# Kernel tuning notes

Measured on AMD Instinct MI355X. Metric: run time of the kernel, lower is better.

The kernel has to match this reference:

```python
import jax, jax.numpy as jnp
import numpy as np

IN_F = 2048
OUT_F = 2048
N_ROWS = 8192


def _perm(n):
    # t_o(n) is a permutation matrix P with P[i, p(i)] = 1, p(i) = (4i mod n) + (4i // n)
    i = np.arange(n)
    return (4 * i) % n + (4 * i) // n


def _inv(p):
    inv = np.empty_like(p)
    inv[p] = np.arange(len(p))
    return inv

# (P_in^T @ H)[a, :] = H[i, :] where p_in(i) = a  ->  rows indexed by inv(p_in)
_INV_P_IN = _inv(_perm(IN_F))
# (H @ P_out)[:, b] = H[:, j] where p_out(j) = b  ->  cols indexed by inv(p_out)
_INV_P_OUT = _inv(_perm(OUT_F))


def make_quaternion_mul(kernel):
    # kernel: (in//4, out); split along dim 1 into quaternion components
    r, i, j, k = jnp.split(kernel, 4, axis=1)
    r2 = jnp.concatenate([r, -i, -j, -k], axis=1)
    i2 = jnp.concatenate([i, r, -k, j], axis=1)
    j2 = jnp.concatenate([j, k, r, -i], axis=1)
    k2 = jnp.concatenate([k, -j, i, r], axis=1)
    return jnp.concatenate([r2, i2, j2, k2], axis=0)  # (in, out)


def setup_inputs() -> dict:
    key = jax.random.key(0)
    k1, k2, k3 = jax.random.split(key, 3)
    inp = jax.random.normal(k1, (N_ROWS, IN_F), dtype=jnp.float32)
    weight = jax.random.normal(k2, (IN_F // 4, OUT_F), dtype=jnp.float32) * (1.0 / np.sqrt(IN_F // 4))
    bias = jax.random.normal(k3, (OUT_F,), dtype=jnp.float32) * 0.01
    return {"input": inp, "weight": weight, "bias": bias}


def reference(input, weight, bias):
    hamilton = make_quaternion_mul(weight)                 # (in, out)
    # swap=True: hamilton = L^T @ hamilton @ R, both pure permutations
    hamilton = hamilton[_INV_P_IN][:, _INV_P_OUT]
    support = input @ hamilton + bias[None, :]             # (N, out)
    return support
```

## Files before the change

### kernel.cpp

```cpp
#include <hip/hip_runtime.h>
#include <stdint.h>

#define IN_F 2048
#define OUT_F 2048
#define N_ROWS 8192

#define BM 256
#define BN 256
#define BK 32
#define NT (IN_F / BK)
#define TM_TILES (N_ROWS / BM)
#define TN_TILES (OUT_F / BN)
#define NWG (TM_TILES * TN_TILES)
#define TILE_SHORTS (BM * BK)
#define BUF_SHORTS (2 * TILE_SHORTS)

typedef __bf16 bf16x8 __attribute__((ext_vector_type(8)));
typedef float f32x4 __attribute__((ext_vector_type(4)));
typedef unsigned short ushortx8 __attribute__((ext_vector_type(8)));

__device__ __forceinline__ unsigned short f2bf(float f) {
  unsigned u = __builtin_bit_cast(unsigned, f);
  u += 0x7FFFu + ((u >> 16) & 1u);
  return (unsigned short)(u >> 16);
}

__device__ __forceinline__ void async16(void* lds, const void* g) {
  __builtin_amdgcn_global_load_lds(
      (const __attribute__((address_space(1))) void*)(uintptr_t)g,
      (__attribute__((address_space(3))) void*)(uint32_t)(uintptr_t)lds,
      16, 0, 0);
}

__device__ __forceinline__ bf16x8 ld8(const unsigned short* p) {
  return __builtin_bit_cast(bf16x8, *reinterpret_cast<const ushortx8*>(p));
}

__global__ __launch_bounds__(256) void k_prep(const float* __restrict__ A,
                                              unsigned short* __restrict__ Ab,
                                              const float* __restrict__ W,
                                              unsigned short* __restrict__ Ht) {
  const int bid = blockIdx.x;
  if (bid < 8192) {
    const size_t t = (size_t)bid * 256 + threadIdx.x;
    const float4* a4 = reinterpret_cast<const float4*>(A);
    float4 v0 = a4[2 * t];
    float4 v1 = a4[2 * t + 1];
    ushortx8 o;
    o[0] = f2bf(v0.x); o[1] = f2bf(v0.y); o[2] = f2bf(v0.z); o[3] = f2bf(v0.w);
    o[4] = f2bf(v1.x); o[5] = f2bf(v1.y); o[6] = f2bf(v1.z); o[7] = f2bf(v1.w);
    *reinterpret_cast<ushortx8*>(Ab + t * 8) = o;
  } else {
    const int t = (bid - 8192) * 256 + threadIdx.x;
    const int b = t >> 8;
    const int a0 = (t & 255) << 3;
    const int c = b & 3, v = b >> 2;
    ushortx8 o;
#pragma unroll
    for (int e = 0; e < 8; ++e) {
      const int a = a0 + e;
      const int q = a & 3, u = a >> 2;
      float w = W[(size_t)u * OUT_F + ((q ^ c) << 9) + v];
      if ((0x284E >> ((q << 2) | c)) & 1) w = -w;
      o[e] = f2bf(w);
    }
    *reinterpret_cast<ushortx8*>(Ht + (size_t)b * IN_F + a0) = o;
  }
}

__global__ __launch_bounds__(512, 2) void k_gemm(const unsigned short* __restrict__ A,
                                                 const unsigned short* __restrict__ Bt,
                                                 const float* __restrict__ bias,
                                                 float* __restrict__ C) {
  __shared__ __align__(16) unsigned short lds[4 * BUF_SHORTS];

  const int tid = threadIdx.x;
  const int lane = tid & 63;
  const int w = tid >> 6;
  const int wm = w >> 2;
  const int wn = w & 3;
  const int fr = lane & 15;
  const int g = lane >> 4;

  const int wg = blockIdx.x;
  const int swz = (wg & 7) * (NWG >> 3) + (wg >> 3);
  const int tm = swz >> 3;
  const int tn = swz & 7;
  const int row0 = tm * BM, col0 = tn * BN;

  const unsigned short* srcA[2];
  const unsigned short* srcB[2];
  int tOff[2];
#pragma unroll
  for (int i = 0; i < 2; ++i) {
    const int t = w * 128 + i * 64 + lane;
    const int r = t >> 2, s = t & 3;
    const int ga = s ^ ((r >> 1) & 3);
    srcA[i] = A + (size_t)(row0 + r) * IN_F + ga * 8;
    srcB[i] = Bt + (size_t)(col0 + r) * IN_F + ga * 8;
    tOff[i] = t * 8;
  }

#define STAGE(T)                                              \
  do {                                                        \
    unsigned short* base_ = &lds[((T) & 3) * BUF_SHORTS];     \
    const int ko_ = (T) * BK;                                 \
    async16(base_ + tOff[0], srcA[0] + ko_);                  \
    async16(base_ + tOff[1], srcA[1] + ko_);                  \
    async16(base_ + TILE_SHORTS + tOff[0], srcB[0] + ko_);    \
    async16(base_ + TILE_SHORTS + tOff[1], srcB[1] + ko_);    \
  } while (0)

  int offA[8], offB[4];
#pragma unroll
  for (int m = 0; m < 8; ++m) {
    const int r = wm * 128 + m * 16 + fr;
    offA[m] = r * BK + (g ^ ((r >> 1) & 3)) * 8;
  }
#pragma unroll
  for (int n = 0; n < 4; ++n) {
    const int r = wn * 64 + n * 16 + fr;
    offB[n] = r * BK + (g ^ ((r >> 1) & 3)) * 8;
  }

  f32x4 acc[8][4] = {};

#define MFMA_(a_, b_, c_) __builtin_amdgcn_mfma_f32_16x16x32_bf16(a_, b_, c_, 0, 0, 0)
#define FENCE_ __builtin_amdgcn_sched_barrier(0)

  STAGE(0);
  STAGE(1);
  STAGE(2);

#define TILE(T, VMSTR, DOSTAGE)                                               \
  do {                                                                        \
    asm volatile("s_waitcnt vmcnt(" VMSTR ")" ::: "memory");                  \
    __builtin_amdgcn_s_barrier();                                             \
    FENCE_;                                                                   \
    const unsigned short* ab_ = &lds[((T) & 3) * BUF_SHORTS];                 \
    const unsigned short* bb_ = ab_ + TILE_SHORTS;                            \
    bf16x8 bg[4], af0[4], af1[4];                                             \
    _Pragma("unroll") for (int n = 0; n < 4; ++n) bg[n] = ld8(bb_ + offB[n]); \
    _Pragma("unroll") for (int m = 0; m < 4; ++m) af0[m] = ld8(ab_ + offA[m]);\
    FENCE_;                                                                   \
    if (DOSTAGE) STAGE((T) + 3);                                              \
    _Pragma("unroll") for (int m = 0; m < 4; ++m)                             \
        af1[m] = ld8(ab_ + offA[4 + m]);                                      \
    FENCE_;                                                                   \
    __builtin_amdgcn_s_setprio(1);                                            \
    _Pragma("unroll") for (int n = 0; n < 4; ++n)                             \
        _Pragma("unroll") for (int m = 0; m < 4; ++m)                         \
            acc[m][n] = MFMA_(af0[m], bg[n], acc[m][n]);                      \
    __builtin_amdgcn_s_setprio(0);                                            \
    FENCE_;                                                                   \
    __builtin_amdgcn_s_setprio(1);                                            \
    _Pragma("unroll") for (int n = 0; n < 4; ++n)                             \
        _Pragma("unroll") for (int m = 0; m < 4; ++m)                         \
            acc[4 + m][n] = MFMA_(af1[m], bg[n], acc[4 + m][n]);              \
    __builtin_amdgcn_s_setprio(0);                                            \
    FENCE_;                                                                   \
  } while (0)

  for (int t = 0; t < NT - 3; ++t) {
    TILE(t, "8", true);
  }
  TILE(NT - 3, "8", false);
  TILE(NT - 2, "4", false);
  TILE(NT - 1, "0", false);

#undef TILE
#undef STAGE

  const int g4 = g << 2;
  float bv[4];
#pragma unroll
  for (int n = 0; n < 4; ++n) bv[n] = bias[col0 + wn * 64 + n * 16 + fr];
#pragma unroll
  for (int m = 0; m < 8; ++m) {
#pragma unroll
    for (int e = 0; e < 4; ++e) {
      const int row = row0 + wm * 128 + m * 16 + g4 + e;
      float* cp = C + (size_t)row * OUT_F + col0 + wn * 64 + fr;
#pragma unroll
      for (int n = 0; n < 4; ++n) cp[n * 16] = acc[m][n][e] + bv[n];
    }
  }
}

__global__ __launch_bounds__(256) void k_naive(const float* __restrict__ A,
                                               const float* __restrict__ W,
                                               const float* __restrict__ bias,
                                               float* __restrict__ C) {
  const int idx = blockIdx.x * 256 + threadIdx.x;
  const int m = idx >> 11;
  const int b = idx & (OUT_F - 1);
  const int c = b & 3, v = b >> 2;
  float acc = 0.f;
  const float* arow = A + (size_t)m * IN_F;
  for (int a = 0; a < IN_F; ++a) {
    const int q = a & 3, u = a >> 2;
    float h = W[(size_t)u * OUT_F + ((q ^ c) << 9) + v];
    if ((0x284E >> ((q << 2) | c)) & 1) h = -h;
    acc += arow[a] * h;
  }
  C[idx] = acc + bias[b];
}

extern "C" void kernel_launch(void* const* d_in, const int* in_sizes, int n_in,
                              void* d_out, int out_size, void* d_ws, size_t ws_size,
                              hipStream_t stream) {
  (void)in_sizes; (void)n_in; (void)out_size;
  const float* inp  = (const float*)d_in[0];
  const float* w    = (const float*)d_in[1];
  const float* bias = (const float*)d_in[2];
  float* out = (float*)d_out;

  const size_t needA = (size_t)N_ROWS * IN_F * sizeof(unsigned short);
  const size_t needH = (size_t)IN_F * OUT_F * sizeof(unsigned short);
  if (ws_size < needA + needH) {
    k_naive<<<(N_ROWS * OUT_F) / 256, 256, 0, stream>>>(inp, w, bias, out);
    return;
  }

  unsigned short* Ab = (unsigned short*)d_ws;
  unsigned short* Ht = Ab + (size_t)N_ROWS * IN_F;

  k_prep<<<8192 + 2048, 256, 0, stream>>>(inp, Ab, w, Ht);
  k_gemm<<<NWG, 512, 0, stream>>>(Ab, Ht, bias, out);
}
```

Baseline: 97.15 us.

## Restructure GEMM main loop into BK=64 ping-pong with interleaved half-tile staging

Doubles the K tile to 64 and replaces the 4-deep ring of small stages with two LDS buffers. Each iteration reads fragments in quarter-M slices and issues the next tile's A/B halves between them, using a new 8-way XOR swizzle for the wider rows. Barriers separate every read/MFMA phase so that global loads overlap compute at a finer grain. The trade is many more workgroup barriers per iteration and a shallower prefetch, which could expose memory latency.

```diff
diff --git a/kernel.cpp b/kernel.cpp
--- a/kernel.cpp
+++ b/kernel.cpp
@@ -7,13 +7,13 @@
 
 #define BM 256
 #define BN 256
-#define BK 32
+#define BK 64
 #define NT (IN_F / BK)
 #define TM_TILES (N_ROWS / BM)
 #define TN_TILES (OUT_F / BN)
 #define NWG (TM_TILES * TN_TILES)
-#define TILE_SHORTS (BM * BK)
-#define BUF_SHORTS (2 * TILE_SHORTS)
+#define AB_STRIDE 32768
+#define B_OFF 16384
 
 typedef __bf16 bf16x8 __attribute__((ext_vector_type(8)));
 typedef float f32x4 __attribute__((ext_vector_type(4)));
@@ -72,7 +72,7 @@
                                                  const unsigned short* __restrict__ Bt,
                                                  const float* __restrict__ bias,
                                                  float* __restrict__ C) {
-  __shared__ __align__(16) unsigned short lds[4 * BUF_SHORTS];
+  __shared__ __align__(16) unsigned short lds[2 * AB_STRIDE];
 
   const int tid = threadIdx.x;
   const int lane = tid & 63;
@@ -88,88 +88,111 @@
   const int tn = swz & 7;
   const int row0 = tm * BM, col0 = tn * BN;
 
-  const unsigned short* srcA[2];
-  const unsigned short* srcB[2];
-  int tOff[2];
-#pragma unroll
-  for (int i = 0; i < 2; ++i) {
-    const int t = w * 128 + i * 64 + lane;
-    const int r = t >> 2, s = t & 3;
-    const int ga = s ^ ((r >> 1) & 3);
-    srcA[i] = A + (size_t)(row0 + r) * IN_F + ga * 8;
-    srcB[i] = Bt + (size_t)(col0 + r) * IN_F + ga * 8;
-    tOff[i] = t * 8;
-  }
-
-#define STAGE(T)                                              \
-  do {                                                        \
-    unsigned short* base_ = &lds[((T) & 3) * BUF_SHORTS];     \
-    const int ko_ = (T) * BK;                                 \
-    async16(base_ + tOff[0], srcA[0] + ko_);                  \
-    async16(base_ + tOff[1], srcA[1] + ko_);                  \
-    async16(base_ + TILE_SHORTS + tOff[0], srcB[0] + ko_);    \
-    async16(base_ + TILE_SHORTS + tOff[1], srcB[1] + ko_);    \
+  const int kgsw = (((tid & 7) ^ ((tid >> 3) & 7)) << 3);
+  const unsigned short* srcA0 = A + (size_t)(row0 + (tid >> 3)) * IN_F + kgsw;
+  const unsigned short* srcB0 = Bt + (size_t)(col0 + (tid >> 3)) * IN_F + kgsw;
+
+#define STG_A(P, H, T)                                                      \
+  do {                                                                      \
+    unsigned short* d_ = lds + (P) * AB_STRIDE + (H) * 8192 + tid * 8;      \
+    const unsigned short* s_ = srcA0 + (size_t)(H) * 128 * IN_F + (T) * BK; \
+    async16(d_, s_);                                                        \
+    async16(d_ + 4096, s_ + (size_t)64 * IN_F);                             \
   } while (0)
-
-  int offA[8], offB[4];
-#pragma unroll
-  for (int m = 0; m < 8; ++m) {
-    const int r = wm * 128 + m * 16 + fr;
-    offA[m] = r * BK + (g ^ ((r >> 1) & 3)) * 8;
-  }
-#pragma unroll
-  for (int n = 0; n < 4; ++n) {
-    const int r = wn * 64 + n * 16 + fr;
-    offB[n] = r * BK + (g ^ ((r >> 1) & 3)) * 8;
-  }
+#define STG_B(P, H, T)                                                        \
+  do {                                                                        \
+    unsigned short* d_ = lds + (P) * AB_STRIDE + B_OFF + (H) * 8192 + tid * 8;\
+    const unsigned short* s_ = srcB0 + (size_t)(H) * 128 * IN_F + (T) * BK;   \
+    async16(d_, s_);                                                          \
+    async16(d_ + 4096, s_ + (size_t)64 * IN_F);                               \
+  } while (0)
+
+  int slot[2];
+#pragma unroll
+  for (int kh = 0; kh < 2; ++kh) slot[kh] = (((g + 4 * kh) ^ (fr & 7)) << 3);
+  int offArow[8], offBrow[4];
+#pragma unroll
+  for (int m = 0; m < 8; ++m) offArow[m] = (wm * 128 + m * 16 + fr) * BK;
+#pragma unroll
+  for (int n = 0; n < 4; ++n) offBrow[n] = (wn * 64 + n * 16 + fr) * BK;
 
   f32x4 acc[8][4] = {};
+  bf16x8 bF[4][2], aF[2][2];
 
 #define MFMA_(a_, b_, c_) __builtin_amdgcn_mfma_f32_16x16x32_bf16(a_, b_, c_, 0, 0, 0)
 #define FENCE_ __builtin_amdgcn_sched_barrier(0)
-
-  STAGE(0);
-  STAGE(1);
-  STAGE(2);
-
-#define TILE(T, VMSTR, DOSTAGE)                                               \
-  do {                                                                        \
-    asm volatile("s_waitcnt vmcnt(" VMSTR ")" ::: "memory");                  \
-    __builtin_amdgcn_s_barrier();                                             \
-    FENCE_;                                                                   \
-    const unsigned short* ab_ = &lds[((T) & 3) * BUF_SHORTS];                 \
-    const unsigned short* bb_ = ab_ + TILE_SHORTS;                            \
-    bf16x8 bg[4], af0[4], af1[4];                                             \
-    _Pragma("unroll") for (int n = 0; n < 4; ++n) bg[n] = ld8(bb_ + offB[n]); \
-    _Pragma("unroll") for (int m = 0; m < 4; ++m) af0[m] = ld8(ab_ + offA[m]);\
-    FENCE_;                                                                   \
-    if (DOSTAGE) STAGE((T) + 3);                                              \
-    _Pragma("unroll") for (int m = 0; m < 4; ++m)                             \
-        af1[m] = ld8(ab_ + offA[4 + m]);                                      \
-    FENCE_;                                                                   \
-    __builtin_amdgcn_s_setprio(1);                                            \
-    _Pragma("unroll") for (int n = 0; n < 4; ++n)                             \
-        _Pragma("unroll") for (int m = 0; m < 4; ++m)                         \
-            acc[m][n] = MFMA_(af0[m], bg[n], acc[m][n]);                      \
-    __builtin_amdgcn_s_setprio(0);                                            \
-    FENCE_;                                                                   \
-    __builtin_amdgcn_s_setprio(1);                                            \
-    _Pragma("unroll") for (int n = 0; n < 4; ++n)                             \
-        _Pragma("unroll") for (int m = 0; m < 4; ++m)                         \
-            acc[4 + m][n] = MFMA_(af1[m], bg[n], acc[4 + m][n]);              \
-    __builtin_amdgcn_s_setprio(0);                                            \
-    FENCE_;                                                                   \
-  } while (0)
-
-  for (int t = 0; t < NT - 3; ++t) {
-    TILE(t, "8", true);
-  }
-  TILE(NT - 3, "8", false);
-  TILE(NT - 2, "4", false);
-  TILE(NT - 1, "0", false);
-
-#undef TILE
-#undef STAGE
+#define BAR_ __builtin_amdgcn_s_barrier()
+#define VM4_ asm volatile("s_waitcnt vmcnt(4)" ::: "memory")
+#define VM0_ asm volatile("s_waitcnt vmcnt(0)" ::: "memory")
+
+#define RD_B(P)                                                               \
+  _Pragma("unroll") for (int n = 0; n < 4; ++n)                               \
+    _Pragma("unroll") for (int kh = 0; kh < 2; ++kh)                          \
+      bF[n][kh] = ld8(lds + (P) * AB_STRIDE + B_OFF + offBrow[n] + slot[kh]);
+#define RD_A(P, M0)                                                           \
+  _Pragma("unroll") for (int e = 0; e < 2; ++e)                               \
+    _Pragma("unroll") for (int kh = 0; kh < 2; ++kh)                          \
+      aF[e][kh] = ld8(lds + (P) * AB_STRIDE + offArow[(M0) + e] + slot[kh]);
+#define DO_MFMA(M0)                                                           \
+  __builtin_amdgcn_s_setprio(1);                                              \
+  _Pragma("unroll") for (int kh = 0; kh < 2; ++kh)                            \
+    _Pragma("unroll") for (int n = 0; n < 4; ++n) {                           \
+      acc[(M0)][n] = MFMA_(aF[0][kh], bF[n][kh], acc[(M0)][n]);               \
+      acc[(M0) + 1][n] = MFMA_(aF[1][kh], bF[n][kh], acc[(M0) + 1][n]);       \
+    }                                                                         \
+  __builtin_amdgcn_s_setprio(0)
+
+  STG_A(0, 0, 0); STG_A(0, 1, 0);
+  STG_B(0, 0, 0); STG_B(0, 1, 0);
+  STG_B(1, 0, 1); STG_B(1, 1, 1);
+  VM0_;
+  BAR_; FENCE_;
+
+#pragma unroll 1
+  for (int i = 0; i < 15; ++i) {
+    const int t1 = 2 * i + 1, t2 = 2 * i + 2, t3 = 2 * i + 3;
+    RD_B(0); RD_A(0, 0); FENCE_; STG_A(1, 0, t1); FENCE_; BAR_; FENCE_;
+    DO_MFMA(0); FENCE_; BAR_; FENCE_;
+    RD_A(0, 2); FENCE_; STG_A(1, 1, t1); FENCE_; BAR_; FENCE_;
+    DO_MFMA(2); FENCE_; BAR_; FENCE_;
+    RD_A(0, 4); FENCE_; STG_B(0, 0, t2); FENCE_; BAR_; FENCE_;
+    DO_MFMA(4); FENCE_; BAR_; FENCE_;
+    RD_A(0, 6); FENCE_; STG_B(0, 1, t2); FENCE_; BAR_; FENCE_;
+    DO_MFMA(6); FENCE_; VM4_; BAR_; FENCE_;
+    RD_B(1); RD_A(1, 0); FENCE_; STG_A(0, 0, t2); FENCE_; BAR_; FENCE_;
+    DO_MFMA(0); FENCE_; BAR_; FENCE_;
+    RD_A(1, 2); FENCE_; STG_A(0, 1, t2); FENCE_; BAR_; FENCE_;
+    DO_MFMA(2); FENCE_; BAR_; FENCE_;
+    RD_A(1, 4); FENCE_; STG_B(1, 0, t3); FENCE_; BAR_; FENCE_;
+    DO_MFMA(4); FENCE_; BAR_; FENCE_;
+    RD_A(1, 6); FENCE_; STG_B(1, 1, t3); FENCE_; BAR_; FENCE_;
+    DO_MFMA(6); FENCE_; VM4_; BAR_; FENCE_;
+  }
+
+  {
+    RD_B(0); RD_A(0, 0); FENCE_; STG_A(1, 0, 31); FENCE_; BAR_; FENCE_;
+    DO_MFMA(0); FENCE_; BAR_; FENCE_;
+    RD_A(0, 2); FENCE_; STG_A(1, 1, 31); FENCE_; BAR_; FENCE_;
+    DO_MFMA(2); FENCE_; BAR_; FENCE_;
+    RD_A(0, 4); FENCE_; BAR_; FENCE_;
+    DO_MFMA(4); FENCE_; BAR_; FENCE_;
+    RD_A(0, 6); FENCE_; BAR_; FENCE_;
+    DO_MFMA(6); FENCE_; VM0_; BAR_; FENCE_;
+    RD_B(1); RD_A(1, 0); FENCE_; BAR_; FENCE_;
+    DO_MFMA(0); FENCE_; BAR_; FENCE_;
+    RD_A(1, 2); FENCE_; BAR_; FENCE_;
+    DO_MFMA(2); FENCE_; BAR_; FENCE_;
+    RD_A(1, 4); FENCE_; BAR_; FENCE_;
+    DO_MFMA(4); FENCE_; BAR_; FENCE_;
+    RD_A(1, 6); FENCE_; BAR_; FENCE_;
+    DO_MFMA(6); FENCE_;
+  }
+
+#undef RD_B
+#undef RD_A
+#undef DO_MFMA
+#undef STG_A
+#undef STG_B
 
   const int g4 = g << 2;
   float bv[4];
```

Result: faster. 94.31 us (-2.9%).

## Interleave LDS fragment reads with MFMAs using register double-buffered B fragments

Applied to the files above, without the earlier changes.

Restructures the GEMM main loop so that each k-step splits its MFMAs into four groups of eight. The LDS reads for the next A fragments, and for the next tile's B fragments, are issued between those groups using inline ds_read_b128 and explicit lgkmcnt waits. B fragments are ping-ponged between two register sets, and the next tile's first A fragments are prefetched before the last MFMA group. The aim is to hide LDS read latency behind matrix math instead of loading all fragments up front. In exchange it uses a vmcnt(0) wait each step, which drains all outstanding global-to-LDS loads and may reduce the effective prefetch depth. It also adds register pressure and relies on hand-placed wait counts.

```diff
diff --git a/kernel.cpp b/kernel.cpp
--- a/kernel.cpp
+++ b/kernel.cpp
@@ -32,8 +32,10 @@
       16, 0, 0);
 }
 
-__device__ __forceinline__ bf16x8 ld8(const unsigned short* p) {
-  return __builtin_bit_cast(bf16x8, *reinterpret_cast<const ushortx8*>(p));
+__device__ __forceinline__ bf16x8 dsr(uint32_t addr) {
+  bf16x8 r;
+  asm volatile("ds_read_b128 %0, %1" : "=v"(r) : "v"(addr));
+  return r;
 }
 
 __global__ __launch_bounds__(256) void k_prep(const float* __restrict__ A,
@@ -88,87 +90,123 @@
   const int tn = swz & 7;
   const int row0 = tm * BM, col0 = tn * BN;
 
-  const unsigned short* srcA[2];
-  const unsigned short* srcB[2];
-  int tOff[2];
-#pragma unroll
-  for (int i = 0; i < 2; ++i) {
-    const int t = w * 128 + i * 64 + lane;
-    const int r = t >> 2, s = t & 3;
-    const int ga = s ^ ((r >> 1) & 3);
-    srcA[i] = A + (size_t)(row0 + r) * IN_F + ga * 8;
-    srcB[i] = Bt + (size_t)(col0 + r) * IN_F + ga * 8;
-    tOff[i] = t * 8;
+  const unsigned short* srcA0;
+  const unsigned short* srcA1;
+  const unsigned short* srcB0;
+  const unsigned short* srcB1;
+  int tOff0, tOff1;
+  {
+    const int t0 = w * 128 + lane, t1 = t0 + 64;
+    const int r0_ = t0 >> 2, s0_ = t0 & 3, ga0 = s0_ ^ ((r0_ >> 1) & 3);
+    const int r1_ = t1 >> 2, s1_ = t1 & 3, ga1 = s1_ ^ ((r1_ >> 1) & 3);
+    srcA0 = A + (size_t)(row0 + r0_) * IN_F + ga0 * 8;
+    srcA1 = A + (size_t)(row0 + r1_) * IN_F + ga1 * 8;
+    srcB0 = Bt + (size_t)(col0 + r0_) * IN_F + ga0 * 8;
+    srcB1 = Bt + (size_t)(col0 + r1_) * IN_F + ga1 * 8;
+    tOff0 = t0 * 8;
+    tOff1 = t1 * 8;
   }
 
 #define STAGE(T)                                              \
   do {                                                        \
     unsigned short* base_ = &lds[((T) & 3) * BUF_SHORTS];     \
     const int ko_ = (T) * BK;                                 \
-    async16(base_ + tOff[0], srcA[0] + ko_);                  \
-    async16(base_ + tOff[1], srcA[1] + ko_);                  \
-    async16(base_ + TILE_SHORTS + tOff[0], srcB[0] + ko_);    \
-    async16(base_ + TILE_SHORTS + tOff[1], srcB[1] + ko_);    \
+    async16(base_ + tOff0, srcA0 + ko_);                      \
+    async16(base_ + tOff1, srcA1 + ko_);                      \
+    async16(base_ + TILE_SHORTS + tOff0, srcB0 + ko_);        \
+    async16(base_ + TILE_SHORTS + tOff1, srcB1 + ko_);        \
   } while (0)
 
-  int offA[8], offB[4];
+  const uint32_t lb = (uint32_t)(uintptr_t)&lds[0];
+  uint32_t aoff[8], boff[4];
 #pragma unroll
   for (int m = 0; m < 8; ++m) {
     const int r = wm * 128 + m * 16 + fr;
-    offA[m] = r * BK + (g ^ ((r >> 1) & 3)) * 8;
+    aoff[m] = (uint32_t)((r * BK + ((g ^ ((r >> 1) & 3)) << 3)) * 2);
   }
 #pragma unroll
   for (int n = 0; n < 4; ++n) {
     const int r = wn * 64 + n * 16 + fr;
-    offB[n] = r * BK + (g ^ ((r >> 1) & 3)) * 8;
+    boff[n] = (uint32_t)(TILE_SHORTS * 2 + (r * BK + ((g ^ ((r >> 1) & 3)) << 3)) * 2);
   }
 
   f32x4 acc[8][4] = {};
+  bf16x8 aP[2], aQ[2], bX[4], bY[4];
 
 #define MFMA_(a_, b_, c_) __builtin_amdgcn_mfma_f32_16x16x32_bf16(a_, b_, c_, 0, 0, 0)
 #define FENCE_ __builtin_amdgcn_sched_barrier(0)
+#define SBAR_ asm volatile("s_barrier" ::: "memory")
+#define LGKM3_ asm volatile("s_waitcnt lgkmcnt(3)")
+#define LGKM0_ asm volatile("s_waitcnt lgkmcnt(0)" ::: "memory")
+#define VM0_ asm volatile("s_waitcnt vmcnt(0)" ::: "memory")
+#define VM4_ asm volatile("s_waitcnt vmcnt(4)" ::: "memory")
+
+#define MM8(M0, AP_, B_)                                          \
+  __builtin_amdgcn_s_setprio(1);                                  \
+  acc[(M0)][0] = MFMA_(AP_[0], B_[0], acc[(M0)][0]);              \
+  acc[(M0) + 1][0] = MFMA_(AP_[1], B_[0], acc[(M0) + 1][0]);      \
+  acc[(M0)][1] = MFMA_(AP_[0], B_[1], acc[(M0)][1]);              \
+  acc[(M0) + 1][1] = MFMA_(AP_[1], B_[1], acc[(M0) + 1][1]);      \
+  acc[(M0)][2] = MFMA_(AP_[0], B_[2], acc[(M0)][2]);              \
+  acc[(M0) + 1][2] = MFMA_(AP_[1], B_[2], acc[(M0) + 1][2]);      \
+  acc[(M0)][3] = MFMA_(AP_[0], B_[3], acc[(M0)][3]);              \
+  acc[(M0) + 1][3] = MFMA_(AP_[1], B_[3], acc[(M0) + 1][3]);      \
+  __builtin_amdgcn_s_setprio(0)
+
+#define KSTEP(T, BC_, BN_)                                        \
+                                                         \
+  aQ[0] = dsr(lb + (((T) & 3) << 15) + aoff[2]);                  \
+  aQ[1] = dsr(lb + (((T) & 3) << 15) + aoff[3]);                  \
+  BN_[0] = dsr(lb + ((((T) + 1) & 3) << 15) + boff[0]);           \
+  FENCE_; LGKM3_; FENCE_;                                         \
+  MM8(0, aP, BC_); FENCE_;                                        \
+                                                         \
+  aP[0] = dsr(lb + (((T) & 3) << 15) + aoff[4]);                  \
+  aP[1] = dsr(lb + (((T) & 3) << 15) + aoff[5]);                  \
+  BN_[1] = dsr(lb + ((((T) + 1) & 3) << 15) + boff[1]);           \
+  FENCE_; LGKM3_; FENCE_;                                         \
+  MM8(2, aQ, BC_); FENCE_;                                        \
+                                                         \
+  aQ[0] = dsr(lb + (((T) & 3) << 15) + aoff[6]);                  \
+  aQ[1] = dsr(lb + (((T) & 3) << 15) + aoff[7]);                  \
+  BN_[2] = dsr(lb + ((((T) + 1) & 3) << 15) + boff[2]);           \
+  FENCE_; LGKM3_; FENCE_;                                         \
+  MM8(4, aP, BC_); FENCE_;                                        \
+   \
+   \
+  VM0_; SBAR_; FENCE_;                                            \
+  aP[0] = dsr(lb + ((((T) + 1) & 3) << 15) + aoff[0]);            \
+  aP[1] = dsr(lb + ((((T) + 1) & 3) << 15) + aoff[1]);            \
+  BN_[3] = dsr(lb + ((((T) + 1) & 3) << 15) + boff[3]);           \
+  FENCE_;                                                         \
+  if ((T) + 3 < NT) STAGE((T) + 3);                               \
+  FENCE_; LGKM3_; FENCE_;                                         \
+  MM8(6, aQ, BC_); FENCE_
 
   STAGE(0);
   STAGE(1);
   STAGE(2);
-
-#define TILE(T, VMSTR, DOSTAGE)                                               \
-  do {                                                                        \
-    asm volatile("s_waitcnt vmcnt(" VMSTR ")" ::: "memory");                  \
-    __builtin_amdgcn_s_barrier();                                             \
-    FENCE_;                                                                   \
-    const unsigned short* ab_ = &lds[((T) & 3) * BUF_SHORTS];                 \
-    const unsigned short* bb_ = ab_ + TILE_SHORTS;                            \
-    bf16x8 bg[4], af0[4], af1[4];                                             \
-    _Pragma("unroll") for (int n = 0; n < 4; ++n) bg[n] = ld8(bb_ + offB[n]); \
-    _Pragma("unroll") for (int m = 0; m < 4; ++m) af0[m] = ld8(ab_ + offA[m]);\
-    FENCE_;                                                                   \
-    if (DOSTAGE) STAGE((T) + 3);                                              \
-    _Pragma("unroll") for (int m = 0; m < 4; ++m)                             \
-        af1[m] = ld8(ab_ + offA[4 + m]);                                      \
-    FENCE_;                                                                   \
-    __builtin_amdgcn_s_setprio(1);                                            \
-    _Pragma("unroll") for (int n = 0; n < 4; ++n)                             \
-        _Pragma("unroll") for (int m = 0; m < 4; ++m)                         \
-            acc[m][n] = MFMA_(af0[m], bg[n], acc[m][n]);                      \
-    __builtin_amdgcn_s_setprio(0);                                            \
-    FENCE_;                                                                   \
-    __builtin_amdgcn_s_setprio(1);                                            \
-    _Pragma("unroll") for (int n = 0; n < 4; ++n)                             \
-        _Pragma("unroll") for (int m = 0; m < 4; ++m)                         \
-            acc[4 + m][n] = MFMA_(af1[m], bg[n], acc[4 + m][n]);              \
-    __builtin_amdgcn_s_setprio(0);                                            \
-    FENCE_;                                                                   \
-  } while (0)
-
-  for (int t = 0; t < NT - 3; ++t) {
-    TILE(t, "8", true);
-  }
-  TILE(NT - 3, "8", false);
-  TILE(NT - 2, "4", false);
-  TILE(NT - 1, "0", false);
-
-#undef TILE
+  VM4_; SBAR_; FENCE_;
+  aP[0] = dsr(lb + aoff[0]);
+  aP[1] = dsr(lb + aoff[1]);
+  bX[0] = dsr(lb + boff[0]);
+  bX[1] = dsr(lb + boff[1]);
+  bX[2] = dsr(lb + boff[2]);
+  bX[3] = dsr(lb + boff[3]);
+  FENCE_;
+
+#pragma unroll 1
+  for (int t = 0; t < NT; t += 2) {
+    KSTEP(t, bX, bY);
+    KSTEP(t + 1, bY, bX);
+  }
+
+  LGKM0_; FENCE_;
+  asm volatile("" ::"v"(aP[0]), "v"(aP[1]), "v"(bX[0]), "v"(bX[1]),
+               "v"(bX[2]), "v"(bX[3]));
+
+#undef KSTEP
+#undef MM8
 #undef STAGE
 
   const int g4 = g << 2;
```

Measured after the change: 99.78 us. 1.03x slower.

## Switch GEMM inner loop to 32x32x16 bf16 MFMA tiles

Applied to the files above, without the earlier changes.

Replaces the 16x16x32 MFMA tiling (8x4 fragments per wave) with 32x32x16 MFMA (4x2 fragments, two k-halves). Fewer, larger MFMA instructions cover the same wave tile, which reduces LDS fragment reads per FLOP and issue overhead. It also removes most of the sched_barrier fences that split loads and MFMAs into phases, and keeps the main loop rolled. The epilogue is rewritten to the 32x32 accumulator layout, at the cost of losing the explicit load/compute interleaving that the fences enforced.

```diff
diff --git a/kernel.cpp b/kernel.cpp
--- a/kernel.cpp
+++ b/kernel.cpp
@@ -16,7 +16,7 @@
 #define BUF_SHORTS (2 * TILE_SHORTS)
 
 typedef __bf16 bf16x8 __attribute__((ext_vector_type(8)));
-typedef float f32x4 __attribute__((ext_vector_type(4)));
+typedef float f32x16 __attribute__((ext_vector_type(16)));
 typedef unsigned short ushortx8 __attribute__((ext_vector_type(8)));
 
 __device__ __forceinline__ unsigned short f2bf(float f) {
@@ -79,8 +79,8 @@
   const int w = tid >> 6;
   const int wm = w >> 2;
   const int wn = w & 3;
-  const int fr = lane & 15;
-  const int g = lane >> 4;
+  const int fr32 = lane & 31;
+  const int half = lane >> 5;
 
   const int wg = blockIdx.x;
   const int swz = (wg & 7) * (NWG >> 3) + (wg >> 3);
@@ -111,22 +111,30 @@
     async16(base_ + TILE_SHORTS + tOff[1], srcB[1] + ko_);    \
   } while (0)
 
-  int offA[8], offB[4];
-#pragma unroll
-  for (int m = 0; m < 8; ++m) {
-    const int r = wm * 128 + m * 16 + fr;
-    offA[m] = r * BK + (g ^ ((r >> 1) & 3)) * 8;
-  }
-#pragma unroll
-  for (int n = 0; n < 4; ++n) {
-    const int r = wn * 64 + n * 16 + fr;
-    offB[n] = r * BK + (g ^ ((r >> 1) & 3)) * 8;
-  }
-
-  f32x4 acc[8][4] = {};
-
-#define MFMA_(a_, b_, c_) __builtin_amdgcn_mfma_f32_16x16x32_bf16(a_, b_, c_, 0, 0, 0)
-#define FENCE_ __builtin_amdgcn_sched_barrier(0)
+  int offA32[4][2], offB32[2][2];
+#pragma unroll
+  for (int mi = 0; mi < 4; ++mi) {
+    const int r = wm * 128 + mi * 32 + fr32;
+#pragma unroll
+    for (int kh = 0; kh < 2; ++kh) {
+      const int gk = 2 * kh + half;
+      offA32[mi][kh] = r * BK + ((gk ^ ((r >> 1) & 3)) << 3);
+    }
+  }
+#pragma unroll
+  for (int ni = 0; ni < 2; ++ni) {
+    const int r = wn * 64 + ni * 32 + fr32;
+#pragma unroll
+    for (int kh = 0; kh < 2; ++kh) {
+      const int gk = 2 * kh + half;
+      offB32[ni][kh] = TILE_SHORTS + r * BK + ((gk ^ ((r >> 1) & 3)) << 3);
+    }
+  }
+
+  f32x16 acc[4][2] = {};
+
+#define MFMA32_(a_, b_, c_) \
+  __builtin_amdgcn_mfma_f32_32x32x16_bf16(a_, b_, c_, 0, 0, 0)
 
   STAGE(0);
   STAGE(1);
@@ -136,31 +144,25 @@
   do {                                                                        \
     asm volatile("s_waitcnt vmcnt(" VMSTR ")" ::: "memory");                  \
     __builtin_amdgcn_s_barrier();                                             \
-    FENCE_;                                                                   \
-    const unsigned short* ab_ = &lds[((T) & 3) * BUF_SHORTS];                 \
-    const unsigned short* bb_ = ab_ + TILE_SHORTS;                            \
-    bf16x8 bg[4], af0[4], af1[4];                                             \
-    _Pragma("unroll") for (int n = 0; n < 4; ++n) bg[n] = ld8(bb_ + offB[n]); \
-    _Pragma("unroll") for (int m = 0; m < 4; ++m) af0[m] = ld8(ab_ + offA[m]);\
-    FENCE_;                                                                   \
+    __builtin_amdgcn_sched_barrier(0);                                        \
+    const unsigned short* b_ = &lds[((T) & 3) * BUF_SHORTS];                  \
+    bf16x8 bf[2][2], af[4][2];                                                \
+    _Pragma("unroll") for (int ni = 0; ni < 2; ++ni)                          \
+      _Pragma("unroll") for (int kh = 0; kh < 2; ++kh)                        \
+        bf[ni][kh] = ld8(b_ + offB32[ni][kh]);                                \
+    _Pragma("unroll") for (int mi = 0; mi < 4; ++mi)                          \
+      _Pragma("unroll") for (int kh = 0; kh < 2; ++kh)                        \
+        af[mi][kh] = ld8(b_ + offA32[mi][kh]);                                \
     if (DOSTAGE) STAGE((T) + 3);                                              \
-    _Pragma("unroll") for (int m = 0; m < 4; ++m)                             \
-        af1[m] = ld8(ab_ + offA[4 + m]);                                      \
-    FENCE_;                                                                   \
     __builtin_amdgcn_s_setprio(1);                                            \
-    _Pragma("unroll") for (int n = 0; n < 4; ++n)                             \
-        _Pragma("unroll") for (int m = 0; m < 4; ++m)                         \
-            acc[m][n] = MFMA_(af0[m], bg[n], acc[m][n]);                      \
+    _Pragma("unroll") for (int kh = 0; kh < 2; ++kh)                          \
+      _Pragma("unroll") for (int mi = 0; mi < 4; ++mi)                        \
+        _Pragma("unroll") for (int ni = 0; ni < 2; ++ni)                      \
+          acc[mi][ni] = MFMA32_(af[mi][kh], bf[ni][kh], acc[mi][ni]);         \
     __builtin_amdgcn_s_setprio(0);                                            \
-    FENCE_;                                                                   \
-    __builtin_amdgcn_s_setprio(1);                                            \
-    _Pragma("unroll") for (int n = 0; n < 4; ++n)                             \
-        _Pragma("unroll") for (int m = 0; m < 4; ++m)                         \
-            acc[4 + m][n] = MFMA_(af1[m], bg[n], acc[4 + m][n]);              \
-    __builtin_amdgcn_s_setprio(0);                                            \
-    FENCE_;                                                                   \
   } while (0)
 
+#pragma unroll 1
   for (int t = 0; t < NT - 3; ++t) {
     TILE(t, "8", true);
   }
@@ -171,18 +173,19 @@
 #undef TILE
 #undef STAGE
 
-  const int g4 = g << 2;
-  float bv[4];
-#pragma unroll
-  for (int n = 0; n < 4; ++n) bv[n] = bias[col0 + wn * 64 + n * 16 + fr];
-#pragma unroll
-  for (int m = 0; m < 8; ++m) {
-#pragma unroll
-    for (int e = 0; e < 4; ++e) {
-      const int row = row0 + wm * 128 + m * 16 + g4 + e;
-      float* cp = C + (size_t)row * OUT_F + col0 + wn * 64 + fr;
-#pragma unroll
-      for (int n = 0; n < 4; ++n) cp[n * 16] = acc[m][n][e] + bv[n];
+  float bv[2];
+#pragma unroll
+  for (int ni = 0; ni < 2; ++ni) bv[ni] = bias[col0 + wn * 64 + ni * 32 + fr32];
+#pragma unroll
+  for (int mi = 0; mi < 4; ++mi) {
+#pragma unroll
+    for (int ni = 0; ni < 2; ++ni) {
+#pragma unroll
+      for (int reg = 0; reg < 16; ++reg) {
+        const int row = row0 + wm * 128 + mi * 32 + (reg & 3) + 8 * (reg >> 2) + 4 * half;
+        const int col = col0 + wn * 64 + ni * 32 + fr32;
+        C[(size_t)row * OUT_F + col] = acc[mi][ni][reg] + bv[ni];
+      }
     }
   }
 }
```

Result: slower. 104.9 us (+8.0%).
